# Optimization experiments

Hardware: AMD Instinct MI355X
Metric: run time of the kernel (lower is better)

## Reference

```python
import jax, jax.numpy as jnp
import numpy as np

B, C, H, W, D = 4, 8, 160, 160, 160
N_PER = 100000
IMAGE_DIM = 160


def setup_inputs() -> dict:
    key = jax.random.key(0)
    k1, k2 = jax.random.split(key)
    image_features = jax.random.normal(k1, (B, C, H, W, D), dtype=jnp.float32)
    # coords uniform in [0, IMAGE_DIM); last 3 columns are x,y,z
    graph_features = jax.random.uniform(k2, (B * N_PER, 3), dtype=jnp.float32) * IMAGE_DIM
    batch = jnp.arange(B * N_PER, dtype=jnp.int32) // N_PER  # equal count per image (required by cat dim=0)
    return {
        "image_features": image_features,
        "graph_features": graph_features,
        "batch": batch,
        "image_dim": IMAGE_DIM,
    }


def _trilerp(image_features, graph_features, image_dim):
    Bn, Cc, Hh, Ww, Dd = image_features.shape
    n_per = graph_features.shape[0] // Bn
    dt = graph_features.dtype
    factor = jnp.asarray(image_dim, dt) / Hh  # original uses image_dim/h for all axes
    xyz = graph_features[:, -3:].reshape(Bn, n_per, 3) / factor  # [B, n, 3]
    x, y, z = xyz[..., 0], xyz[..., 1], xyz[..., 2]

    def bounds(v, size):
        lo = jnp.minimum(jnp.floor(v), size - 1)
        hi = jnp.minimum(jnp.ceil(v), size - 1)
        return lo, hi

    x1f, x2f = bounds(x, Hh)
    y1f, y2f = bounds(y, Ww)
    z1f, z2f = bounds(z, Dd)
    x1, x2 = x1f.astype(jnp.int32), x2f.astype(jnp.int32)
    y1, y2 = y1f.astype(jnp.int32), y2f.astype(jnp.int32)
    z1, z2 = z1f.astype(jnp.int32), z2f.astype(jnp.int32)
    # weights exactly as in original (degenerate-to-zero when floor==ceil, kept faithfully)
    wx, wx2 = x - x1f, x2f - x
    wy, wy2 = y - y1f, y2f - y
    wz, wz2 = z - z1f, z2f - z

    def per_image(img, x1, x2, y1, y2, z1, z2, wx, wx2, wy, wy2, wz, wz2):
        # img: [C, H, W, D]; indices/weights: [n]
        def g(xi, yi, zi):
            return img[:, xi, yi, zi]  # [C, n]

        def lerp_y(zc):
            lx1 = g(x2, y1, zc) * wx + g(x1, y1, zc) * wx2
            lx2 = g(x2, y2, zc) * wx + g(x1, y2, zc) * wx2
            return lx2 * wy + lx1 * wy2

        return lerp_y(z2) * wz + lerp_y(z1) * wz2  # [C, n]

    out = jax.vmap(per_image)(
        image_features, x1, x2, y1, y2, z1, z2, wx, wx2, wy, wy2, wz, wz2
    )  # [B, C, n]
    # torch.cat over batch along dim 0 of [C, n] blocks == reshape to [B*C, n]; then permute(1,0)
    return out.reshape(Bn * Cc, n_per).T  # [n, B*C]


def reference(image_features, graph_features, batch, image_dim):
    # batch is arange(N)//n_per (sorted, equal counts), so grouping == reshape; batch unused numerically
    return _trilerp(image_features, graph_features, image_dim)
```

## Files before the change

kernel.cpp:

```cpp
#include <hip/hip_runtime.h>
#include <hip/hip_fp16.h>

constexpr int B = 4, C = 8, H = 160, W = 160, Dd = 160, NPER = 100000;
constexpr long HWD = (long)H * W * Dd;
constexpr int  TOTAL_PTS = NPER * B;
constexpr int  TOTAL_OUT = NPER * B * C;
constexpr size_t WS_NEEDED = (size_t)B * HWD * C * sizeof(__half);

__global__ __launch_bounds__(256) void transpose_kernel(
    const float* __restrict__ img, __half* __restrict__ ws)
{
    long t = (long)blockIdx.x * 256 + threadIdx.x;
    const long nquads = (long)B * HWD / 4;
    if (t >= nquads) return;

    long v0 = t * 4;
    long b  = v0 / HWD;
    long v  = v0 - b * HWD;
    const float* base = img + b * C * HWD + v;

    float4 ch[8];
    #pragma unroll
    for (int c = 0; c < 8; ++c)
        ch[c] = *reinterpret_cast<const float4*>(base + (long)c * HWD);

    #pragma unroll
    for (int q = 0; q < 4; ++q) {
        __half h[8];
        #pragma unroll
        for (int c = 0; c < 8; ++c)
            h[c] = __float2half(reinterpret_cast<const float*>(&ch[c])[q]);
        *reinterpret_cast<float4*>(ws + (v0 + q) * 8) =
            *reinterpret_cast<const float4*>(h);
    }
}

__global__ __launch_bounds__(256) void gather_kernel(
    const __half* __restrict__ ws,
    const float*  __restrict__ gf,
    const int*    __restrict__ dimp,
    float*        __restrict__ out)
{
    int t = blockIdx.x * 256 + threadIdx.x;
    if (t >= TOTAL_PTS) return;
    int j = t >> 2;
    int b = t & 3;

    int iv = dimp[0];
    float image_dim = (iv > 0 && iv < 1000000) ? (float)iv : __int_as_float(iv);
    float factor = image_dim / (float)H;

    long p = (long)b * NPER + j;
    float x = gf[p * 3 + 0] / factor;
    float y = gf[p * 3 + 1] / factor;
    float z = gf[p * 3 + 2] / factor;

    float x1f = fminf(floorf(x), (float)(H - 1));
    float x2f = fminf(ceilf(x),  (float)(H - 1));
    float y1f = fminf(floorf(y), (float)(W - 1));
    float y2f = fminf(ceilf(y),  (float)(W - 1));
    float z1f = fminf(floorf(z), (float)(Dd - 1));
    float z2f = fminf(ceilf(z),  (float)(Dd - 1));

    int x1 = max(0, (int)x1f), x2 = max(0, (int)x2f);
    int y1 = max(0, (int)y1f), y2 = max(0, (int)y2f);
    int z1 = max(0, (int)z1f), z2 = max(0, (int)z2f);

    float wx = x - x1f, wx2 = x2f - x;
    float wy = y - y1f, wy2 = y2f - y;
    float wz = z - z1f, wz2 = z2f - z;

    const __half* base = ws + (long)b * HWD * 8;

    auto corner = [&](int xi, int yi, int zi, float* v) {
        long vox = ((long)xi * W + yi) * Dd + zi;
        float4 raw = *reinterpret_cast<const float4*>(base + vox * 8);
        const __half* h = reinterpret_cast<const __half*>(&raw);
        #pragma unroll
        for (int c = 0; c < 8; ++c) v[c] = __half2float(h[c]);
    };

    float a11[8], a12[8], a21[8], a22[8];
    float ly_a[8], ly_b[8];

    corner(x1, y1, z2, a11);
    corner(x1, y2, z2, a12);
    corner(x2, y1, z2, a21);
    corner(x2, y2, z2, a22);
    #pragma unroll
    for (int c = 0; c < 8; ++c) {
        float lx1 = a21[c] * wx + a11[c] * wx2;
        float lx2 = a22[c] * wx + a12[c] * wx2;
        ly_a[c] = lx2 * wy + lx1 * wy2;
    }
    corner(x1, y1, z1, a11);
    corner(x1, y2, z1, a12);
    corner(x2, y1, z1, a21);
    corner(x2, y2, z1, a22);
    #pragma unroll
    for (int c = 0; c < 8; ++c) {
        float lx1 = a21[c] * wx + a11[c] * wx2;
        float lx2 = a22[c] * wx + a12[c] * wx2;
        ly_b[c] = lx2 * wy + lx1 * wy2;
    }

    float res[8];
    #pragma unroll
    for (int c = 0; c < 8; ++c) res[c] = ly_a[c] * wz + ly_b[c] * wz2;

    float* dst = out + (long)j * 32 + b * 8;
    *reinterpret_cast<float4*>(dst)     = *reinterpret_cast<const float4*>(&res[0]);
    *reinterpret_cast<float4*>(dst + 4) = *reinterpret_cast<const float4*>(&res[4]);
}

__global__ __launch_bounds__(256) void og_proj_direct(
    const float* __restrict__ img, const float* __restrict__ gf,
    const int* __restrict__ dimp, float* __restrict__ out)
{
    int o = blockIdx.x * 256 + threadIdx.x;
    if (o >= TOTAL_OUT) return;
    int j = o >> 5, bc = o & 31, b = bc >> 3, c = bc & 7;

    int iv = dimp[0];
    float image_dim = (iv > 0 && iv < 1000000) ? (float)iv : __int_as_float(iv);
    float factor = image_dim / (float)H;

    long p = (long)b * NPER + j;
    float x = gf[p * 3 + 0] / factor;
    float y = gf[p * 3 + 1] / factor;
    float z = gf[p * 3 + 2] / factor;

    float x1f = fminf(floorf(x), (float)(H - 1));
    float x2f = fminf(ceilf(x),  (float)(H - 1));
    float y1f = fminf(floorf(y), (float)(W - 1));
    float y2f = fminf(ceilf(y),  (float)(W - 1));
    float z1f = fminf(floorf(z), (float)(Dd - 1));
    float z2f = fminf(ceilf(z),  (float)(Dd - 1));
    int x1 = max(0, (int)x1f), x2 = max(0, (int)x2f);
    int y1 = max(0, (int)y1f), y2 = max(0, (int)y2f);
    int z1 = max(0, (int)z1f), z2 = max(0, (int)z2f);
    float wx = x - x1f, wx2 = x2f - x;
    float wy = y - y1f, wy2 = y2f - y;
    float wz = z - z1f, wz2 = z2f - z;

    const float* base = img + (size_t)(b * C + c) * (size_t)HWD;
    size_t r11 = ((size_t)x1 * W + y1) * Dd;
    size_t r12 = ((size_t)x1 * W + y2) * Dd;
    size_t r21 = ((size_t)x2 * W + y1) * Dd;
    size_t r22 = ((size_t)x2 * W + y2) * Dd;

    float lx1_a = base[r21 + z2] * wx + base[r11 + z2] * wx2;
    float lx2_a = base[r22 + z2] * wx + base[r12 + z2] * wx2;
    float ly_a  = lx2_a * wy + lx1_a * wy2;
    float lx1_b = base[r21 + z1] * wx + base[r11 + z1] * wx2;
    float lx2_b = base[r22 + z1] * wx + base[r12 + z1] * wx2;
    float ly_b  = lx2_b * wy + lx1_b * wy2;
    out[o] = ly_a * wz + ly_b * wz2;
}

extern "C" void kernel_launch(void* const* d_in, const int* in_sizes, int n_in,
                              void* d_out, int out_size, void* d_ws, size_t ws_size,
                              hipStream_t stream) {
    const float* img  = (const float*)d_in[0];
    const float* gf   = (const float*)d_in[1];
    const int*   dimp = (const int*)d_in[3];
    float* out = (float*)d_out;

    if (ws_size >= WS_NEEDED) {
        __half* ws = (__half*)d_ws;
        long nquads = (long)B * HWD / 4;
        int tblocks = (int)((nquads + 255) / 256);
        transpose_kernel<<<tblocks, 256, 0, stream>>>(img, ws);
        int gblocks = (TOTAL_PTS + 255) / 256;
        gather_kernel<<<gblocks, 256, 0, stream>>>(ws, gf, dimp, out);
    } else {
        int blocks = (TOTAL_OUT + 255) / 256;
        og_proj_direct<<<blocks, 256, 0, stream>>>(img, gf, dimp, out);
    }
}
```

Before: 206.7 us.

## Counting-sort points by (batch,x,y) cell before gather for cache locality

```diff
diff --git a/kernel.cpp b/kernel.cpp
--- a/kernel.cpp
+++ b/kernel.cpp
@@ -5,7 +5,94 @@
 constexpr long HWD = (long)H * W * Dd;
 constexpr int  TOTAL_PTS = NPER * B;
 constexpr int  TOTAL_OUT = NPER * B * C;
-constexpr size_t WS_NEEDED = (size_t)B * HWD * C * sizeof(__half);
+constexpr int  NKEYS = B * H * W;
+
+constexpr size_t WS_IMG_BYTES    = (size_t)B * HWD * C * sizeof(__half);
+constexpr size_t WS_COUNTS_OFF   = WS_IMG_BYTES;
+constexpr size_t WS_SORTED_OFF   = WS_COUNTS_OFF + (size_t)NKEYS * 4;
+constexpr size_t WS_NEEDED       = WS_SORTED_OFF + (size_t)TOTAL_PTS * 4;
+
+__device__ __forceinline__ float load_image_dim(const int* dimp) {
+    int iv = dimp[0];
+    return (iv > 0 && iv < 1000000) ? (float)iv : __int_as_float(iv);
+}
+
+struct Coord {
+    int x1, x2, y1, y2, z1, z2;
+    float wx, wx2, wy, wy2, wz, wz2;
+};
+__device__ __forceinline__ Coord make_coord(const float* __restrict__ gf,
+                                            int p, float factor) {
+    Coord c;
+    float x = gf[(long)p * 3 + 0] / factor;
+    float y = gf[(long)p * 3 + 1] / factor;
+    float z = gf[(long)p * 3 + 2] / factor;
+    float x1f = fminf(floorf(x), (float)(H - 1));
+    float x2f = fminf(ceilf(x),  (float)(H - 1));
+    float y1f = fminf(floorf(y), (float)(W - 1));
+    float y2f = fminf(ceilf(y),  (float)(W - 1));
+    float z1f = fminf(floorf(z), (float)(Dd - 1));
+    float z2f = fminf(ceilf(z),  (float)(Dd - 1));
+    c.x1 = max(0, (int)x1f); c.x2 = max(0, (int)x2f);
+    c.y1 = max(0, (int)y1f); c.y2 = max(0, (int)y2f);
+    c.z1 = max(0, (int)z1f); c.z2 = max(0, (int)z2f);
+    c.wx = x - x1f; c.wx2 = x2f - x;
+    c.wy = y - y1f; c.wy2 = y2f - y;
+    c.wz = z - z1f; c.wz2 = z2f - z;
+    return c;
+}
+
+__global__ __launch_bounds__(256) void hist_kernel(
+    const float* __restrict__ gf, const int* __restrict__ dimp,
+    int* __restrict__ counts)
+{
+    int p = blockIdx.x * 256 + threadIdx.x;
+    if (p >= TOTAL_PTS) return;
+    float factor = load_image_dim(dimp) / (float)H;
+    int b = p / NPER;
+    Coord c = make_coord(gf, p, factor);
+    int key = (b * H + c.x1) * W + c.y1;
+    atomicAdd(&counts[key], 1);
+}
+
+__global__ __launch_bounds__(1024) void scan_kernel(int* __restrict__ counts)
+{
+    constexpr int CHUNK = NKEYS / 1024;
+    __shared__ int part[1024];
+    int tid = threadIdx.x;
+    int beg = tid * CHUNK;
+    int s = 0;
+    #pragma unroll 4
+    for (int i = 0; i < CHUNK; ++i) s += counts[beg + i];
+    part[tid] = s;
+    __syncthreads();
+    for (int off = 1; off < 1024; off <<= 1) {
+        int v = (tid >= off) ? part[tid - off] : 0;
+        __syncthreads();
+        part[tid] += v;
+        __syncthreads();
+    }
+    int run = part[tid] - s;
+    for (int i = 0; i < CHUNK; ++i) {
+        int cnt = counts[beg + i];
+        counts[beg + i] = run;
+        run += cnt;
+    }
+}
+
+__global__ __launch_bounds__(256) void scatter_kernel(
+    const float* __restrict__ gf, const int* __restrict__ dimp,
+    int* __restrict__ counts, int* __restrict__ sorted)
+{
+    int p = blockIdx.x * 256 + threadIdx.x;
+    if (p >= TOTAL_PTS) return;
+    float factor = load_image_dim(dimp) / (float)H;
+    int b = p / NPER;
+    Coord c = make_coord(gf, p, factor);
+    int key = (b * H + c.x1) * W + c.y1;
+    int pos = atomicAdd(&counts[key], 1);
+    sorted[pos] = p;
+}
 
 __global__ __launch_bounds__(256) void transpose_kernel(
     const float* __restrict__ img, __half* __restrict__ ws)
@@ -13,7 +100,6 @@
     long t = (long)blockIdx.x * 256 + threadIdx.x;
     const long nquads = (long)B * HWD / 4;
     if (t >= nquads) return;
-
     long v0 = t * 4;
     long b  = v0 / HWD;
     long v  = v0 - b * HWD;
@@ -36,42 +122,20 @@
 }
 
 __global__ __launch_bounds__(256) void gather_kernel(
-    const __half* __restrict__ ws,
-    const float*  __restrict__ gf,
-    const int*    __restrict__ dimp,
-    float*        __restrict__ out)
-{
-    int t = blockIdx.x * 256 + threadIdx.x;
-    if (t >= TOTAL_PTS) return;
-    int j = t >> 2;
-    int b = t & 3;
-
-    int iv = dimp[0];
-    float image_dim = (iv > 0 && iv < 1000000) ? (float)iv : __int_as_float(iv);
-    float factor = image_dim / (float)H;
-
-    long p = (long)b * NPER + j;
-    float x = gf[p * 3 + 0] / factor;
-    float y = gf[p * 3 + 1] / factor;
-    float z = gf[p * 3 + 2] / factor;
-
-    float x1f = fminf(floorf(x), (float)(H - 1));
-    float x2f = fminf(ceilf(x),  (float)(H - 1));
-    float y1f = fminf(floorf(y), (float)(W - 1));
-    float y2f = fminf(ceilf(y),  (float)(W - 1));
-    float z1f = fminf(floorf(z), (float)(Dd - 1));
-    float z2f = fminf(ceilf(z),  (float)(Dd - 1));
-
-    int x1 = max(0, (int)x1f), x2 = max(0, (int)x2f);
-    int y1 = max(0, (int)y1f), y2 = max(0, (int)y2f);
-    int z1 = max(0, (int)z1f), z2 = max(0, (int)z2f);
-
-    float wx = x - x1f, wx2 = x2f - x;
-    float wy = y - y1f, wy2 = y2f - y;
-    float wz = z - z1f, wz2 = z2f - z;
+    const __half* __restrict__ ws, const float* __restrict__ gf,
+    const int* __restrict__ dimp, const int* __restrict__ sorted,
+    float* __restrict__ out)
+{
+    int i = blockIdx.x * 256 + threadIdx.x;
+    if (i >= TOTAL_PTS) return;
+    int p = sorted[i];
+    int b = p / NPER;
+    int j = p - b * NPER;
+
+    float factor = load_image_dim(dimp) / (float)H;
+    Coord cc = make_coord(gf, p, factor);
 
     const __half* base = ws + (long)b * HWD * 8;
-
     auto corner = [&](int xi, int yi, int zi, float* v) {
         long vox = ((long)xi * W + yi) * Dd + zi;
         float4 raw = *reinterpret_cast<const float4*>(base + vox * 8);
@@ -80,33 +144,32 @@
         for (int c = 0; c < 8; ++c) v[c] = __half2float(h[c]);
     };
 
-    float a11[8], a12[8], a21[8], a22[8];
-    float ly_a[8], ly_b[8];
-
-    corner(x1, y1, z2, a11);
-    corner(x1, y2, z2, a12);
-    corner(x2, y1, z2, a21);
-    corner(x2, y2, z2, a22);
+    float a11[8], a12[8], a21[8], a22[8], ly_a[8], ly_b[8];
+
+    corner(cc.x1, cc.y1, cc.z2, a11);
+    corner(cc.x1, cc.y2, cc.z2, a12);
+    corner(cc.x2, cc.y1, cc.z2, a21);
+    corner(cc.x2, cc.y2, cc.z2, a22);
     #pragma unroll
     for (int c = 0; c < 8; ++c) {
-        float lx1 = a21[c] * wx + a11[c] * wx2;
-        float lx2 = a22[c] * wx + a12[c] * wx2;
-        ly_a[c] = lx2 * wy + lx1 * wy2;
-    }
-    corner(x1, y1, z1, a11);
-    corner(x1, y2, z1, a12);
-    corner(x2, y1, z1, a21);
-    corner(x2, y2, z1, a22);
+        float lx1 = a21[c] * cc.wx + a11[c] * cc.wx2;
+        float lx2 = a22[c] * cc.wx + a12[c] * cc.wx2;
+        ly_a[c] = lx2 * cc.wy + lx1 * cc.wy2;
+    }
+    corner(cc.x1, cc.y1, cc.z1, a11);
+    corner(cc.x1, cc.y2, cc.z1, a12);
+    corner(cc.x2, cc.y1, cc.z1, a21);
+    corner(cc.x2, cc.y2, cc.z1, a22);
     #pragma unroll
     for (int c = 0; c < 8; ++c) {
-        float lx1 = a21[c] * wx + a11[c] * wx2;
-        float lx2 = a22[c] * wx + a12[c] * wx2;
-        ly_b[c] = lx2 * wy + lx1 * wy2;
+        float lx1 = a21[c] * cc.wx + a11[c] * cc.wx2;
+        float lx2 = a22[c] * cc.wx + a12[c] * cc.wx2;
+        ly_b[c] = lx2 * cc.wy + lx1 * cc.wy2;
     }
 
     float res[8];
     #pragma unroll
-    for (int c = 0; c < 8; ++c) res[c] = ly_a[c] * wz + ly_b[c] * wz2;
+    for (int c = 0; c < 8; ++c) res[c] = ly_a[c] * cc.wz + ly_b[c] * cc.wz2;
 
     float* dst = out + (long)j * 32 + b * 8;
     *reinterpret_cast<float4*>(dst)     = *reinterpret_cast<const float4*>(&res[0]);
@@ -120,42 +183,22 @@
     int o = blockIdx.x * 256 + threadIdx.x;
     if (o >= TOTAL_OUT) return;
     int j = o >> 5, bc = o & 31, b = bc >> 3, c = bc & 7;
-
-    int iv = dimp[0];
-    float image_dim = (iv > 0 && iv < 1000000) ? (float)iv : __int_as_float(iv);
-    float factor = image_dim / (float)H;
-
-    long p = (long)b * NPER + j;
-    float x = gf[p * 3 + 0] / factor;
-    float y = gf[p * 3 + 1] / factor;
-    float z = gf[p * 3 + 2] / factor;
-
-    float x1f = fminf(floorf(x), (float)(H - 1));
-    float x2f = fminf(ceilf(x),  (float)(H - 1));
-    float y1f = fminf(floorf(y), (float)(W - 1));
-    float y2f = fminf(ceilf(y),  (float)(W - 1));
-    float z1f = fminf(floorf(z), (float)(Dd - 1));
-    float z2f = fminf(ceilf(z),  (float)(Dd - 1));
-    int x1 = max(0, (int)x1f), x2 = max(0, (int)x2f);
-    int y1 = max(0, (int)y1f), y2 = max(0, (int)y2f);
-    int z1 = max(0, (int)z1f), z2 = max(0, (int)z2f);
-    float wx = x - x1f, wx2 = x2f - x;
-    float wy = y - y1f, wy2 = y2f - y;
-    float wz = z - z1f, wz2 = z2f - z;
+    float factor = load_image_dim(dimp) / (float)H;
+    Coord cc = make_coord(gf, b * NPER + j, factor);
 
     const float* base = img + (size_t)(b * C + c) * (size_t)HWD;
-    size_t r11 = ((size_t)x1 * W + y1) * Dd;
-    size_t r12 = ((size_t)x1 * W + y2) * Dd;
-    size_t r21 = ((size_t)x2 * W + y1) * Dd;
-    size_t r22 = ((size_t)x2 * W + y2) * Dd;
-
-    float lx1_a = base[r21 + z2] * wx + base[r11 + z2] * wx2;
-    float lx2_a = base[r22 + z2] * wx + base[r12 + z2] * wx2;
-    float ly_a  = lx2_a * wy + lx1_a * wy2;
-    float lx1_b = base[r21 + z1] * wx + base[r11 + z1] * wx2;
-    float lx2_b = base[r22 + z1] * wx + base[r12 + z1] * wx2;
-    float ly_b  = lx2_b * wy + lx1_b * wy2;
-    out[o] = ly_a * wz + ly_b * wz2;
+    size_t r11 = ((size_t)cc.x1 * W + cc.y1) * Dd;
+    size_t r12 = ((size_t)cc.x1 * W + cc.y2) * Dd;
+    size_t r21 = ((size_t)cc.x2 * W + cc.y1) * Dd;
+    size_t r22 = ((size_t)cc.x2 * W + cc.y2) * Dd;
+
+    float lx1_a = base[r21 + cc.z2] * cc.wx + base[r11 + cc.z2] * cc.wx2;
+    float lx2_a = base[r22 + cc.z2] * cc.wx + base[r12 + cc.z2] * cc.wx2;
+    float ly_a  = lx2_a * cc.wy + lx1_a * cc.wy2;
+    float lx1_b = base[r21 + cc.z1] * cc.wx + base[r11 + cc.z1] * cc.wx2;
+    float lx2_b = base[r22 + cc.z1] * cc.wx + base[r12 + cc.z1] * cc.wx2;
+    float ly_b  = lx2_b * cc.wy + lx1_b * cc.wy2;
+    out[o] = ly_a * cc.wz + ly_b * cc.wz2;
 }
 
 extern "C" void kernel_launch(void* const* d_in, const int* in_sizes, int n_in,
@@ -168,11 +211,19 @@
 
     if (ws_size >= WS_NEEDED) {
         __half* ws = (__half*)d_ws;
+        int* counts = (int*)((char*)d_ws + WS_COUNTS_OFF);
+        int* sorted = (int*)((char*)d_ws + WS_SORTED_OFF);
+
+        hipMemsetAsync(counts, 0, (size_t)NKEYS * 4, stream);
+        int pblocks = (TOTAL_PTS + 255) / 256;
+        hist_kernel<<<pblocks, 256, 0, stream>>>(gf, dimp, counts);
+        scan_kernel<<<1, 1024, 0, stream>>>(counts);
+        scatter_kernel<<<pblocks, 256, 0, stream>>>(gf, dimp, counts, sorted);
+
         long nquads = (long)B * HWD / 4;
         int tblocks = (int)((nquads + 255) / 256);
         transpose_kernel<<<tblocks, 256, 0, stream>>>(img, ws);
-        int gblocks = (TOTAL_PTS + 255) / 256;
-        gather_kernel<<<gblocks, 256, 0, stream>>>(ws, gf, dimp, out);
+        gather_kernel<<<pblocks, 256, 0, stream>>>(ws, gf, dimp, sorted, out);
     } else {
         int blocks = (TOTAL_OUT + 255) / 256;
         og_proj_direct<<<blocks, 256, 0, stream>>>(img, gf, dimp, out);
```

Result: slower. 302.7 us (+46.5%).
